# Kernel optimization log

Hardware: AMD Instinct MI355X
Metric: run time of the kernel (lower is better)

## Reference

```python
import jax, jax.numpy as jnp
import numpy as np

EPS = 1e-08

def rms_norm(x, eps=EPS):
    # Matches torch: mean-centered, population variance (unbiased=False)
    mean = jnp.mean(x, axis=-1, keepdims=True)
    var = jnp.var(x, axis=-1, keepdims=True)
    return (x - mean) / jnp.sqrt(var + eps)

def activation_quant(x):
    s = 127.0 / jnp.max(jnp.abs(x), axis=-1, keepdims=True)
    return jnp.clip(jnp.round(s * x), -128, 127) / s

def ternary_matmul(x, w):
    # pos_mask - neg_mask of sign(w) equals sign(w); x @ sign(w).T
    return jnp.matmul(x, jnp.sign(w).T)

def setup_inputs() -> dict:
    key = jax.random.key(0)
    k0, k1, k2, k3 = jax.random.split(key, 4)
    B, S, D, H = 4, 2048, 2048, 8192
    x = jax.random.normal(k0, (B, S, D), dtype=jnp.float32)
    W_g = jax.random.normal(k1, (H, D), dtype=jnp.float32) * 0.01
    W_u = jax.random.normal(k2, (H, D), dtype=jnp.float32) * 0.01
    W_d = jax.random.normal(k3, (D, H), dtype=jnp.float32) * 0.01
    return {"x": x, "W_g": W_g, "W_u": W_u, "W_d": W_d}

def reference(x, W_g, W_u, W_d):
    xq = activation_quant(rms_norm(x))
    g = jax.nn.silu(ternary_matmul(xq, W_g))   # [B,S,H]
    u = ternary_matmul(xq, W_u)                # [B,S,H]
    p = g * u
    return ternary_matmul(p, W_d)              # [B,S,D]
```

## Files before the change

kernel.cpp:

```cpp
#include <hip/hip_runtime.h>
#include <stdint.h>

#define MROWS 8192
#define DDIM  2048
#define HDIM  8192

typedef __attribute__((ext_vector_type(8))) short bf16x8;
typedef __attribute__((ext_vector_type(4))) float f32x4;
typedef __attribute__((ext_vector_type(4))) int   i32x4;
typedef unsigned short u16;

__device__ __forceinline__ void async_load16(const void* g, void* l) {
  auto gp = reinterpret_cast<const __attribute__((address_space(1))) unsigned int*>(
      reinterpret_cast<uintptr_t>(g));
  auto lp = reinterpret_cast<__attribute__((address_space(3))) unsigned int*>(
      reinterpret_cast<uintptr_t>(l));
  __builtin_amdgcn_global_load_lds(gp, lp, 16, 0, 0);
}

__device__ __forceinline__ u16 f2bf(float f) {
  union { float f; unsigned int u; } v; v.f = f;
  unsigned int r = v.u + 0x7FFF + ((v.u >> 16) & 1);
  return (u16)(r >> 16);
}

__global__ void sign_i8x2_kernel(const float* __restrict__ wg, const float* __restrict__ wu,
                                 char* __restrict__ og, char* __restrict__ ou) {
  const int t = blockIdx.x * 256 + threadIdx.x;
  const float* w = blockIdx.y ? wu : wg;
  char* o = blockIdx.y ? ou : og;
  const float4* w4 = (const float4*)w;
  float4 a = w4[t * 2], b = w4[t * 2 + 1];
  float v[8] = {a.x, a.y, a.z, a.w, b.x, b.y, b.z, b.w};
  union { char s[8]; uint2 u; } pk;
#pragma unroll
  for (int i = 0; i < 8; i++)
    pk.s[i] = v[i] > 0.f ? (char)1 : (v[i] < 0.f ? (char)-1 : (char)0);
  ((uint2*)o)[t] = pk.u;
}

__global__ void sign_bf16_kernel(const float* __restrict__ w, u16* __restrict__ o) {
  const int t = blockIdx.x * 256 + threadIdx.x;
  const float4* w4 = (const float4*)w;
  float4 a = w4[t * 2], b = w4[t * 2 + 1];
  float v[8] = {a.x, a.y, a.z, a.w, b.x, b.y, b.z, b.w};
  union { u16 s[8]; uint4 u; } pk;
#pragma unroll
  for (int i = 0; i < 8; i++)
    pk.s[i] = v[i] > 0.f ? 0x3F80 : (v[i] < 0.f ? 0xBF80 : 0);
  ((uint4*)o)[t] = pk.u;
}

__global__ void norm_quant_i8_kernel(const float* __restrict__ x,
                                     char* __restrict__ q, float* __restrict__ inv) {
  const int row  = blockIdx.x;
  const int tid  = threadIdx.x;
  const int lane = tid & 63, wave = tid >> 6;
  const float4* xr = (const float4*)(x + (size_t)row * DDIM);
  float4 a = xr[tid * 2], b = xr[tid * 2 + 1];
  float v[8] = {a.x, a.y, a.z, a.w, b.x, b.y, b.z, b.w};
  float s1 = 0.f, s2 = 0.f;
#pragma unroll
  for (int i = 0; i < 8; i++) { s1 += v[i]; s2 += v[i] * v[i]; }
#pragma unroll
  for (int o = 1; o < 64; o <<= 1) { s1 += __shfl_xor(s1, o); s2 += __shfl_xor(s2, o); }
  __shared__ float ssum[4], ssq[4], smax[4];
  if (lane == 0) { ssum[wave] = s1; ssq[wave] = s2; }
  __syncthreads();
  s1 = ssum[0] + ssum[1] + ssum[2] + ssum[3];
  s2 = ssq[0] + ssq[1] + ssq[2] + ssq[3];
  const float mean = s1 * (1.f / DDIM);
  const float var  = s2 * (1.f / DDIM) - mean * mean;
  const float rstd = rsqrtf(var + 1e-8f);
  float mx = 0.f;
#pragma unroll
  for (int i = 0; i < 8; i++) { v[i] = (v[i] - mean) * rstd; mx = fmaxf(mx, fabsf(v[i])); }
#pragma unroll
  for (int o = 1; o < 64; o <<= 1) mx = fmaxf(mx, __shfl_xor(mx, o));
  if (lane == 0) smax[wave] = mx;
  __syncthreads();
  mx = fmaxf(fmaxf(smax[0], smax[1]), fmaxf(smax[2], smax[3]));
  const float s = 127.f / mx;
  if (tid == 0) inv[row] = mx * (1.f / 127.f);
  union { char s8[8]; uint2 u; } pk;
#pragma unroll
  for (int i = 0; i < 8; i++) {
    float qq = rintf(v[i] * s);
    qq = fminf(fmaxf(qq, -128.f), 127.f);
    pk.s8[i] = (char)(int)qq;
  }
  ((uint2*)(q + (size_t)row * DDIM))[tid] = pk.u;
}

__global__ __launch_bounds__(256, 2) void gemm_glu_i8_kernel(
    const char* __restrict__ A,
    const char* __restrict__ Bg,
    const char* __restrict__ Bu,
    const float* __restrict__ inv,
    u16* __restrict__ P)
{
  constexpr int K = DDIM;
  const int l   = blockIdx.x + gridDim.x * blockIdx.y;
  const int xcd = l & 7;
  const int s_  = l >> 3;
  const int n0 = (xcd * 8 + (s_ & 7)) * 128;
  const int m0 = (s_ >> 3) * 128;
  const int tid  = threadIdx.x;
  const int lane = tid & 63, wave = tid >> 6;
  const int wm = wave >> 1, wn = wave & 1;
  const int quad = lane >> 4, l16 = lane & 15;

  __shared__ __align__(16) char lds[49152];
  char* lA  = lds;
  char* lBg = lds + 16384;
  char* lBu = lds + 32768;

  i32x4 accg[4][4], accu[4][4];
  const i32x4 zero = {0, 0, 0, 0};
#pragma unroll
  for (int i = 0; i < 4; i++)
#pragma unroll
    for (int j = 0; j < 4; j++) { accg[i][j] = zero; accu[i][j] = zero; }

  const int arow = wm * 64 + l16;
  const int brow = wn * 64 + l16;
  const int aswz = (arow & 7) << 4;
  const int bswz = (brow & 7) << 4;

  for (int k0 = 0; k0 < K; k0 += 128) {
    __syncthreads();
#pragma unroll
    for (int is = 0; is < 4; ++is) {
      const int o   = is * 4096 + tid * 16;
      const int r   = o >> 7;
      const int cbs = (o & 127) ^ ((r & 7) << 4);
      async_load16(A  + (size_t)(m0 + r) * K + k0 + cbs, lA  + is * 4096 + wave * 1024);
      async_load16(Bg + (size_t)(n0 + r) * K + k0 + cbs, lBg + is * 4096 + wave * 1024);
      async_load16(Bu + (size_t)(n0 + r) * K + k0 + cbs, lBu + is * 4096 + wave * 1024);
    }
    __syncthreads();
#pragma unroll
    for (int ks = 0; ks < 2; ++ks) {
      const int koff = ks * 64 + quad * 16;
      i32x4 a[4], bg[4], bu[4];
#pragma unroll
      for (int i = 0; i < 4; i++)
        a[i] = *(const i32x4*)(lA + (arow + i * 16) * 128 + (koff ^ aswz));
#pragma unroll
      for (int j = 0; j < 4; j++) {
        bg[j] = *(const i32x4*)(lBg + (brow + j * 16) * 128 + (koff ^ bswz));
        bu[j] = *(const i32x4*)(lBu + (brow + j * 16) * 128 + (koff ^ bswz));
      }
#pragma unroll
      for (int i = 0; i < 4; i++)
#pragma unroll
        for (int j = 0; j < 4; j++) {
          accg[i][j] = __builtin_amdgcn_mfma_i32_16x16x64_i8(a[i], bg[j], accg[i][j], 0, 0, 0);
          accu[i][j] = __builtin_amdgcn_mfma_i32_16x16x64_i8(a[i], bu[j], accu[i][j], 0, 0, 0);
        }
    }
  }

  const int rbase = m0 + wm * 64 + quad * 4;
  const int cbase = n0 + wn * 64 + l16;
#pragma unroll
  for (int i = 0; i < 4; i++) {
    float iv[4];
#pragma unroll
    for (int r = 0; r < 4; r++) iv[r] = inv[rbase + i * 16 + r];
#pragma unroll
    for (int j = 0; j < 4; j++)
#pragma unroll
      for (int r = 0; r < 4; r++) {
        float g = (float)accg[i][j][r] * iv[r];
        float u = (float)accu[i][j][r] * iv[r];
        float pv = (g / (1.f + __expf(-g))) * u;
        P[(size_t)(rbase + i * 16 + r) * HDIM + (cbase + j * 16)] = f2bf(pv);
      }
  }
}

__global__ __launch_bounds__(512, 2) void gemm_out_kernel(
    const u16* __restrict__ A,
    const u16* __restrict__ B,
    float* __restrict__ C)
{
  constexpr size_t KB = (size_t)HDIM * 2;
  constexpr int NT = (int)(KB / 128);
  const int l   = blockIdx.x + gridDim.x * blockIdx.y;
  const int xcd = l & 7;
  const int s_  = l >> 3;
  const int n0 = ((xcd & 1) * 4 + (s_ & 3)) * 256;
  const int m0 = ((xcd >> 1) * 8 + (s_ >> 2)) * 256;
  const int tid  = threadIdx.x;
  const int lane = tid & 63, wave = tid >> 6;
  const int wm = wave >> 2, wn = wave & 3;
  const int quad = lane >> 4, l16 = lane & 15;

  __shared__ __align__(16) char lds[131072];

  f32x4 acc[8][4];
  const f32x4 zero = {0.f, 0.f, 0.f, 0.f};
#pragma unroll
  for (int i = 0; i < 8; i++)
#pragma unroll
    for (int j = 0; j < 4; j++) acc[i][j] = zero;

  const int arow = wm * 128 + l16;
  const int brow = wn * 64 + l16;
  const int swz  = (l16 & 7) << 4;

  const int rr  = tid >> 3;
  const int cbs = ((tid & 7) << 4) ^ ((rr & 7) << 4);
  const char* aSrc = (const char*)A + (size_t)(m0 + rr) * KB + cbs;
  const char* bSrc = (const char*)B + (size_t)(n0 + rr) * KB + cbs;

#define STG2_A(is) async_load16(aSrc + (size_t)(is) * 64 * KB + k0n, bufN + (is) * 8192 + wave * 1024)
#define STG2_B(is) async_load16(bSrc + (size_t)(is) * 64 * KB + k0n, bufN + 32768 + (is) * 8192 + wave * 1024)
#define STG2_TILE() do { STG2_A(0); STG2_A(1); STG2_A(2); STG2_A(3); \
                         STG2_B(0); STG2_B(1); STG2_B(2); STG2_B(3); } while (0)

  {
    char* bufN = lds;           const int k0n = 0;
    STG2_TILE();
  }
  {
    char* bufN = lds + 65536;   const int k0n = 128;
    STG2_TILE();
  }
  asm volatile("s_waitcnt vmcnt(8)" ::: "memory");
  __builtin_amdgcn_s_barrier();

  for (int t = 0; t < NT; ++t) {
    const char* bufC = lds + (size_t)(t & 1) * 65536;
    bf16x8 b[4];
#pragma unroll
    for (int ks = 0; ks < 2; ++ks) {
#pragma unroll
      for (int ih = 0; ih < 2; ++ih) {
        const int koff = (ks * 64 + quad * 16) ^ swz;
        if (ih == 0) {
#pragma unroll
          for (int j = 0; j < 4; ++j)
            b[j] = *(const bf16x8*)(bufC + 32768 + (size_t)(brow + j * 16) * 128 + koff);
        }
        bf16x8 a[4];
#pragma unroll
        for (int ii = 0; ii < 4; ++ii)
          a[ii] = *(const bf16x8*)(bufC + (size_t)(arow + (ih * 4 + ii) * 16) * 128 + koff);
        __builtin_amdgcn_s_barrier();
        __builtin_amdgcn_s_setprio(1);
#pragma unroll
        for (int ii = 0; ii < 4; ++ii) {
          const int i = ih * 4 + ii;
#pragma unroll
          for (int j = 0; j < 4; ++j)
            acc[i][j] = __builtin_amdgcn_mfma_f32_16x16x32_bf16(a[ii], b[j], acc[i][j], 0, 0, 0);
        }
        __builtin_amdgcn_s_setprio(0);
      }
    }
    __builtin_amdgcn_s_barrier();
    if (t + 2 < NT) {
      char* bufN = lds + (size_t)(t & 1) * 65536;
      const int k0n = (t + 2) * 128;
      STG2_TILE();
      asm volatile("s_waitcnt vmcnt(8)" ::: "memory");
    } else {
      asm volatile("s_waitcnt vmcnt(0)" ::: "memory");
    }
    __builtin_amdgcn_s_barrier();
  }
#undef STG2_A
#undef STG2_B
#undef STG2_TILE

  const int rbase = m0 + wm * 128 + quad * 4;
  const int cbase = n0 + wn * 64 + l16;
#pragma unroll
  for (int i = 0; i < 8; i++)
#pragma unroll
    for (int j = 0; j < 4; j++)
#pragma unroll
      for (int r = 0; r < 4; r++)
        C[(size_t)(rbase + i * 16 + r) * DDIM + (cbase + j * 16)] = acc[i][j][r];
}

extern "C" void kernel_launch(void* const* d_in, const int* in_sizes, int n_in,
                              void* d_out, int out_size, void* d_ws, size_t ws_size,
                              hipStream_t stream) {
  const float* x  = (const float*)d_in[0];
  const float* Wg = (const float*)d_in[1];
  const float* Wu = (const float*)d_in[2];
  const float* Wd = (const float*)d_in[3];

  char* ws = (char*)d_ws;
  char*  q    = ws;
  float* inv  = (float*)(ws + 16777216ull);
  char*  sWg  = ws + 20971520ull;
  char*  sWu  = ws + 37748736ull;
  u16*   sWd  = (u16*)(ws + 54525952ull);
  u16*   p    = (u16*)(ws + 88080384ull);
  float* out  = (float*)d_out;

  dim3 gs(8192, 2);
  sign_i8x2_kernel<<<gs, 256, 0, stream>>>(Wg, Wu, sWg, sWu);
  sign_bf16_kernel<<<8192, 256, 0, stream>>>(Wd, sWd);

  norm_quant_i8_kernel<<<MROWS, 256, 0, stream>>>(x, q, inv);

  dim3 g1(HDIM / 128, MROWS / 128);
  gemm_glu_i8_kernel<<<g1, 256, 0, stream>>>(q, sWg, sWu, inv, p);

  dim3 g2(DDIM / 256, MROWS / 256);
  gemm_out_kernel<<<g2, 512, 0, stream>>>(p, sWd, out);
}
```

Baseline: 707.1 us.

## Load GLU weight fragments directly from global into registers, shrink LDS to A only

The gate and up weight tiles are no longer staged through shared memory. Each wave loads its B fragments straight from global memory into registers, software-prefetching the next gate fragment while the current MFMAs run. LDS drops from 48KB to 16KB, which may raise occupancy and removes the LDS read traffic for B. In exchange, B reuse across the two waves sharing a column slice now goes through cache instead of LDS, the global loads are uncoalesced 16-byte reads, and register pressure rises.

```diff
diff --git a/kernel.cpp b/kernel.cpp
--- a/kernel.cpp
+++ b/kernel.cpp
@@ -110,10 +110,7 @@
   const int wm = wave >> 1, wn = wave & 1;
   const int quad = lane >> 4, l16 = lane & 15;
 
-  __shared__ __align__(16) char lds[49152];
-  char* lA  = lds;
-  char* lBg = lds + 16384;
-  char* lBu = lds + 32768;
+  __shared__ __align__(16) char lds[16384];
 
   i32x4 accg[4][4], accu[4][4];
   const i32x4 zero = {0, 0, 0, 0};
@@ -123,9 +120,16 @@
     for (int j = 0; j < 4; j++) { accg[i][j] = zero; accu[i][j] = zero; }
 
   const int arow = wm * 64 + l16;
-  const int brow = wn * 64 + l16;
   const int aswz = (arow & 7) << 4;
-  const int bswz = (brow & 7) << 4;
+
+  const char* gB = Bg + (size_t)(n0 + wn * 64 + l16) * K + quad * 16;
+  const char* uB = Bu + (size_t)(n0 + wn * 64 + l16) * K + quad * 16;
+
+  i32x4 bg_cur[4], bg_nxt[4], bu[4];
+
+#pragma unroll
+  for (int j = 0; j < 4; j++)
+    bg_cur[j] = *(const i32x4*)(gB + (size_t)j * 16 * K);
 
   for (int k0 = 0; k0 < K; k0 += 128) {
     __syncthreads();
@@ -134,30 +138,57 @@
       const int o   = is * 4096 + tid * 16;
       const int r   = o >> 7;
       const int cbs = (o & 127) ^ ((r & 7) << 4);
-      async_load16(A  + (size_t)(m0 + r) * K + k0 + cbs, lA  + is * 4096 + wave * 1024);
-      async_load16(Bg + (size_t)(n0 + r) * K + k0 + cbs, lBg + is * 4096 + wave * 1024);
-      async_load16(Bu + (size_t)(n0 + r) * K + k0 + cbs, lBu + is * 4096 + wave * 1024);
+      async_load16(A + (size_t)(m0 + r) * K + k0 + cbs, lds + is * 4096 + wave * 1024);
     }
     __syncthreads();
-#pragma unroll
-    for (int ks = 0; ks < 2; ++ks) {
-      const int koff = ks * 64 + quad * 16;
-      i32x4 a[4], bg[4], bu[4];
-#pragma unroll
-      for (int i = 0; i < 4; i++)
-        a[i] = *(const i32x4*)(lA + (arow + i * 16) * 128 + (koff ^ aswz));
-#pragma unroll
-      for (int j = 0; j < 4; j++) {
-        bg[j] = *(const i32x4*)(lBg + (brow + j * 16) * 128 + (koff ^ bswz));
-        bu[j] = *(const i32x4*)(lBu + (brow + j * 16) * 128 + (koff ^ bswz));
+
+    {
+#pragma unroll
+      for (int j = 0; j < 4; j++)
+        bu[j] = *(const i32x4*)(uB + (size_t)j * 16 * K + k0);
+#pragma unroll
+      for (int j = 0; j < 4; j++)
+        bg_nxt[j] = *(const i32x4*)(gB + (size_t)j * 16 * K + k0 + 64);
+      i32x4 a[4];
+      const int koff = quad * 16;
+#pragma unroll
+      for (int i = 0; i < 4; i++)
+        a[i] = *(const i32x4*)(lds + (arow + i * 16) * 128 + (koff ^ aswz));
+#pragma unroll
+      for (int i = 0; i < 4; i++)
+#pragma unroll
+        for (int j = 0; j < 4; j++)
+          accg[i][j] = __builtin_amdgcn_mfma_i32_16x16x64_i8(a[i], bg_cur[j], accg[i][j], 0, 0, 0);
+#pragma unroll
+      for (int i = 0; i < 4; i++)
+#pragma unroll
+        for (int j = 0; j < 4; j++)
+          accu[i][j] = __builtin_amdgcn_mfma_i32_16x16x64_i8(a[i], bu[j], accu[i][j], 0, 0, 0);
+    }
+    {
+#pragma unroll
+      for (int j = 0; j < 4; j++)
+        bu[j] = *(const i32x4*)(uB + (size_t)j * 16 * K + k0 + 64);
+      if (k0 + 128 < K) {
+#pragma unroll
+        for (int j = 0; j < 4; j++)
+          bg_cur[j] = *(const i32x4*)(gB + (size_t)j * 16 * K + k0 + 128);
       }
-#pragma unroll
-      for (int i = 0; i < 4; i++)
-#pragma unroll
-        for (int j = 0; j < 4; j++) {
-          accg[i][j] = __builtin_amdgcn_mfma_i32_16x16x64_i8(a[i], bg[j], accg[i][j], 0, 0, 0);
+      i32x4 a[4];
+      const int koff = 64 + quad * 16;
+#pragma unroll
+      for (int i = 0; i < 4; i++)
+        a[i] = *(const i32x4*)(lds + (arow + i * 16) * 128 + (koff ^ aswz));
+#pragma unroll
+      for (int i = 0; i < 4; i++)
+#pragma unroll
+        for (int j = 0; j < 4; j++)
+          accg[i][j] = __builtin_amdgcn_mfma_i32_16x16x64_i8(a[i], bg_nxt[j], accg[i][j], 0, 0, 0);
+#pragma unroll
+      for (int i = 0; i < 4; i++)
+#pragma unroll
+        for (int j = 0; j < 4; j++)
           accu[i][j] = __builtin_amdgcn_mfma_i32_16x16x64_i8(a[i], bu[j], accu[i][j], 0, 0, 0);
-        }
     }
   }
 
```

After: 985.7 us. 39.4% more time.

## Double-buffer B tiles in LDS to overlap loads with MFMA in GLU GEMM

Applied to the files above, without the earlier changes.

Restructures the gate/up int8 GEMM main loop so the Bg/Bu tiles are double-buffered in LDS and prefetched two K-steps ahead, while A stays single-buffered and is loaded one step ahead. Explicit vmcnt waits and raw s_barrier replace the syncthreads pair, so global loads overlap with MFMA work. LDS grows from 48KB to 80KB per block, which may limit how many blocks fit per CU under the launch bounds. The A load for the next step is still issued after compute, so it stays partly exposed.

```diff
diff --git a/kernel.cpp b/kernel.cpp
--- a/kernel.cpp
+++ b/kernel.cpp
@@ -99,7 +99,8 @@
     const float* __restrict__ inv,
     u16* __restrict__ P)
 {
-  constexpr int K = DDIM;
+  constexpr int K  = DDIM;
+  constexpr int NT = K / 128;
   const int l   = blockIdx.x + gridDim.x * blockIdx.y;
   const int xcd = l & 7;
   const int s_  = l >> 3;
@@ -110,10 +111,8 @@
   const int wm = wave >> 1, wn = wave & 1;
   const int quad = lane >> 4, l16 = lane & 15;
 
-  __shared__ __align__(16) char lds[49152];
-  char* lA  = lds;
-  char* lBg = lds + 16384;
-  char* lBu = lds + 32768;
+  __shared__ __align__(16) char lds[81920];
+  char* lA = lds;
 
   i32x4 accg[4][4], accu[4][4];
   const i32x4 zero = {0, 0, 0, 0};
@@ -127,18 +126,27 @@
   const int aswz = (arow & 7) << 4;
   const int bswz = (brow & 7) << 4;
 
-  for (int k0 = 0; k0 < K; k0 += 128) {
-    __syncthreads();
-#pragma unroll
-    for (int is = 0; is < 4; ++is) {
-      const int o   = is * 4096 + tid * 16;
-      const int r   = o >> 7;
-      const int cbs = (o & 127) ^ ((r & 7) << 4);
-      async_load16(A  + (size_t)(m0 + r) * K + k0 + cbs, lA  + is * 4096 + wave * 1024);
-      async_load16(Bg + (size_t)(n0 + r) * K + k0 + cbs, lBg + is * 4096 + wave * 1024);
-      async_load16(Bu + (size_t)(n0 + r) * K + k0 + cbs, lBu + is * 4096 + wave * 1024);
-    }
-    __syncthreads();
+#define STG_A(k0n) do { _Pragma("unroll") for (int is = 0; is < 4; ++is) { \
+    const int o = is * 4096 + tid * 16; const int r = o >> 7; \
+    const int cbs = (o & 127) ^ ((r & 7) << 4); \
+    async_load16(A + (size_t)(m0 + r) * K + (k0n) + cbs, lA + is * 4096 + wave * 1024); } } while (0)
+
+#define STG_B(k0n, bptr) do { _Pragma("unroll") for (int is = 0; is < 4; ++is) { \
+    const int o = is * 4096 + tid * 16; const int r = o >> 7; \
+    const int cbs = (o & 127) ^ ((r & 7) << 4); \
+    async_load16(Bg + (size_t)(n0 + r) * K + (k0n) + cbs, (bptr) + is * 4096 + wave * 1024); \
+    async_load16(Bu + (size_t)(n0 + r) * K + (k0n) + cbs, (bptr) + 16384 + is * 4096 + wave * 1024); } } while (0)
+
+  STG_A(0);
+  STG_B(0,   lds + 16384);
+  STG_B(128, lds + 49152);
+  asm volatile("s_waitcnt vmcnt(8)" ::: "memory");
+  __builtin_amdgcn_s_barrier();
+
+  for (int t = 0; t < NT; ++t) {
+    char* lB = lds + 16384 + (size_t)(t & 1) * 32768;
+    const char* lBg = lB;
+    const char* lBu = lB + 16384;
 #pragma unroll
     for (int ks = 0; ks < 2; ++ks) {
       const int koff = ks * 64 + quad * 16;
@@ -159,7 +167,15 @@
           accu[i][j] = __builtin_amdgcn_mfma_i32_16x16x64_i8(a[i], bu[j], accu[i][j], 0, 0, 0);
         }
     }
-  }
+    __builtin_amdgcn_s_barrier();
+    if (t + 1 < NT) STG_A((t + 1) * 128);
+    if (t + 2 < NT) STG_B((t + 2) * 128, lB);
+    if (t + 2 < NT) asm volatile("s_waitcnt vmcnt(8)" ::: "memory");
+    else            asm volatile("s_waitcnt vmcnt(0)" ::: "memory");
+    __builtin_amdgcn_s_barrier();
+  }
+#undef STG_A
+#undef STG_B
 
   const int rbase = m0 + wm * 64 + quad * 4;
   const int cbase = n0 + wn * 64 + l16;
```

Result: slower. 752.6 us (+6.4%).
